# Optimization experiments

Hardware: AMD Instinct MI355X
Metric: run time of the kernel (lower is better)

The kernel has to match this reference:

```python
import jax, jax.numpy as jnp
import numpy as np

DIM = 768
HEADS = 12
HEAD_DIM = DIM // HEADS
B, N = 8, 1024


def setup_inputs() -> dict:
    key = jax.random.key(0)
    ks = jax.random.split(key, 5)
    x = jax.random.normal(ks[0], (B, N, DIM), dtype=jnp.float32)
    shared_rel_pos = jax.random.normal(ks[1], (HEADS, N, N), dtype=jnp.float32)
    qkv_w = jax.random.normal(ks[2], (3 * DIM, DIM), dtype=jnp.float32) * (DIM ** -0.5)
    proj_w = jax.random.normal(ks[3], (DIM, DIM), dtype=jnp.float32) * (DIM ** -0.5)
    proj_b = jnp.zeros((DIM,), dtype=jnp.float32)
    return {"x": x, "shared_rel_pos": shared_rel_pos, "qkv_w": qkv_w,
            "proj_w": proj_w, "proj_b": proj_b}


def reference(x, shared_rel_pos, qkv_w, proj_w, proj_b):
    Bt, Nt, C = x.shape
    scale = HEAD_DIM ** -0.5
    # qkv: Linear(dim, 3*dim, bias=False) -> (B, N, 3, H, hd) -> (3, B, H, N, hd)
    qkv = jnp.einsum('bnc,oc->bno', x, qkv_w)
    qkv = qkv.reshape(Bt, Nt, 3, HEADS, HEAD_DIM).transpose(2, 0, 3, 1, 4)
    q, k, v = qkv[0], qkv[1], qkv[2]
    # scaled dot-product attention with shared relative-position bias
    attn = jnp.einsum('bhqd,bhkd->bhqk', q, k) * scale
    attn = attn + shared_rel_pos[None]  # broadcast over batch
    attn = jax.nn.softmax(attn, axis=-1)
    out = jnp.einsum('bhqk,bhkd->bhqd', attn, v)
    out = out.transpose(0, 2, 1, 3).reshape(Bt, Nt, C)
    return jnp.einsum('bnc,oc->bno', out, proj_w) + proj_b
```

## Files before the change

kernel.cpp:

```cpp
#include <hip/hip_runtime.h>
#include <hip/hip_bf16.h>
#include <stdint.h>

#define HEADS 12
#define HD 64
#define SEQ 1024
#define CDIM 768

typedef __attribute__((ext_vector_type(8))) short bfrag;
typedef __attribute__((ext_vector_type(4))) float facc;
typedef __attribute__((ext_vector_type(4))) _Float16 h4;

__device__ __forceinline__ ushort f2bf(float f) {
    union { float f; uint32_t u; } v; v.f = f;
    uint32_t u = v.u;
    uint32_t r = (u + 0x7FFFu + ((u >> 16) & 1u)) >> 16;
    return (ushort)r;
}
__device__ __forceinline__ ushort f2h(float f) {
    union { _Float16 h; ushort u; } c; c.h = (_Float16)f; return c.u;
}
__device__ __forceinline__ float h2f(uint32_t u16) {
    union { _Float16 h; ushort u; } c; c.u = (ushort)u16; return (float)c.h;
}

__global__ void cvt_all(const float* __restrict__ x, const float* __restrict__ qw,
                        const float* __restrict__ pw, const float* __restrict__ rel,
                        ushort* __restrict__ xd, ushort* __restrict__ qd,
                        ushort* __restrict__ pd, ushort* __restrict__ rd) {
    long i = ((long)blockIdx.x * 256 + threadIdx.x) * 4;
    if (i < 6291456) {
        float4 v = *(const float4*)(x + i);
        ushort4 o = {f2bf(v.x), f2bf(v.y), f2bf(v.z), f2bf(v.w)};
        *(ushort4*)(xd + i) = o;
    } else if (i < 8060928) {
        long j = i - 6291456;
        float4 v = *(const float4*)(qw + j);
        ushort4 o = {f2bf(v.x), f2bf(v.y), f2bf(v.z), f2bf(v.w)};
        *(ushort4*)(qd + j) = o;
    } else if (i < 8650752) {
        long j = i - 8060928;
        float4 v = *(const float4*)(pw + j);
        ushort4 o = {f2bf(v.x), f2bf(v.y), f2bf(v.z), f2bf(v.w)};
        *(ushort4*)(pd + j) = o;
    } else {
        long j = i - 8650752;
        float4 v = *(const float4*)(rel + j);
        ushort4 o = {f2h(v.x * 1.44269504f), f2h(v.y * 1.44269504f),
                     f2h(v.z * 1.44269504f), f2h(v.w * 1.44269504f)};
        *(ushort4*)(rd + j) = o;
    }
}

#define GLOAD16(gsrc, ldst) \
    __builtin_amdgcn_global_load_lds((const __attribute__((address_space(1))) uint32_t*)(gsrc), \
                                     (__attribute__((address_space(3))) uint32_t*)(ldst), 16, 0, 0)

template<int EPI>
__global__ __launch_bounds__(256) void gemm_nt(
    const ushort* __restrict__ A, const ushort* __restrict__ Bm,
    ushort* __restrict__ qb, ushort* __restrict__ kb, ushort* __restrict__ vb,
    const float* __restrict__ projb, float* __restrict__ out)
{
    __shared__ ushort As[128 * 32];
    __shared__ ushort Bs[128 * 32];
    const int t = threadIdx.x;
    const int w = t >> 6, l = t & 63;
    const int wm = w >> 1, wn = w & 1;
    const int lr = l & 15, lg = l >> 4;
    const int m0 = blockIdx.x * 128;
    const int o0 = blockIdx.y * 128;

    facc acc[4][4] = {};

    const int srow = w * 16 + (l >> 2);
    const int scol = (l & 3) * 8;
    const ushort* Ag = A + (size_t)(m0 + srow) * CDIM + scol;
    const ushort* Bg = Bm + (size_t)(o0 + srow) * CDIM + scol;

    for (int k0 = 0; k0 < CDIM; k0 += 32) {
        __syncthreads();
        GLOAD16(Ag + k0,             As + w * 512);
        GLOAD16(Ag + 64 * CDIM + k0, As + 2048 + w * 512);
        GLOAD16(Bg + k0,             Bs + w * 512);
        GLOAD16(Bg + 64 * CDIM + k0, Bs + 2048 + w * 512);
        __syncthreads();
        bfrag af[4], bf[4];
#pragma unroll
        for (int m = 0; m < 4; ++m)
            af[m] = *(const bfrag*)&As[(wm * 64 + m * 16 + lr) * 32 + lg * 8];
#pragma unroll
        for (int n = 0; n < 4; ++n)
            bf[n] = *(const bfrag*)&Bs[(wn * 64 + n * 16 + lr) * 32 + lg * 8];
#pragma unroll
        for (int m = 0; m < 4; ++m)
#pragma unroll
            for (int n = 0; n < 4; ++n)
                acc[m][n] = __builtin_amdgcn_mfma_f32_16x16x32_bf16(af[m], bf[n], acc[m][n], 0, 0, 0);
    }

    if (EPI == 0) {
        const int tsel = o0 / CDIM;
        const int h_base = (o0 % CDIM) / 64;
        ushort* dst = (tsel == 0) ? qb : ((tsel == 1) ? kb : vb);
        const float scl = (tsel == 0) ? 0.18033688f : 1.0f;
#pragma unroll
        for (int m = 0; m < 4; ++m) {
            int grow = m0 + wm * 64 + m * 16 + lg * 4;
#pragma unroll
            for (int n = 0; n < 4; ++n) {
                int h = h_base + wn;
                int d = n * 16 + lr;
#pragma unroll
                for (int r = 0; r < 4; ++r) {
                    int row = grow + r;
                    int b = row >> 10, nn = row & 1023;
                    ushort val = (tsel == 2) ? f2h(acc[m][n][r])
                                             : f2bf(acc[m][n][r] * scl);
                    dst[(((size_t)(b * HEADS + h)) * SEQ + nn) * HD + d] = val;
                }
            }
        }
    } else {
#pragma unroll
        for (int m = 0; m < 4; ++m) {
            int grow = m0 + wm * 64 + m * 16 + lg * 4;
#pragma unroll
            for (int n = 0; n < 4; ++n) {
                int o = o0 + wn * 64 + n * 16 + lr;
                float bias = projb[o];
#pragma unroll
                for (int r = 0; r < 4; ++r)
                    out[(size_t)(grow + r) * CDIM + o] = acc[m][n][r] + bias;
            }
        }
    }
}

__global__ __launch_bounds__(256, 3) void attn_kernel(
    const ushort* __restrict__ qbuf, const ushort* __restrict__ kbuf,
    const ushort* __restrict__ vbuf, const ushort* __restrict__ biash,
    ushort* __restrict__ attn_out)
{
    __shared__ ushort Ks[2][64 * 72];
    __shared__ ushort Vt[2][64 * 72];

    const int t = threadIdx.x;
    const int w = t >> 6, l = t & 63;
    const int lr = l & 15, lg = l >> 4;

    const int bid = blockIdx.x;
    const int lid = (bid & 7) * 96 + (bid >> 3);
    const int h  = lid >> 6;
    const int qt = (lid >> 3) & 7;
    const int b  = lid & 7;

    const int q0 = qt * 128;
    const size_t headoff = (size_t)(b * HEADS + h) * SEQ * HD;
    const int qrb = q0 + w * 32;

    bfrag aQ[2][2];
#pragma unroll
    for (int n = 0; n < 2; ++n) {
        const ushort* Qp = qbuf + headoff + (size_t)(qrb + n * 16 + lr) * HD;
        aQ[n][0] = *(const bfrag*)(Qp + lg * 8);
        aQ[n][1] = *(const bfrag*)(Qp + 32 + lg * 8);
    }

    float mrun[2] = {-1e30f, -1e30f}, lrun[2] = {0.0f, 0.0f};
    facc Ov[2][4] = {};

    const ushort* bprow[2];
#pragma unroll
    for (int n = 0; n < 2; ++n)
        bprow[n] = biash + ((size_t)h * SEQ + qrb + n * 16 + lr) * SEQ;

    const int krow = t >> 3, kc = (t & 7) * 8;
    const int p2 = t & 31, vg_ = t >> 5;
    const ushort* kgb = kbuf + headoff + (size_t)krow * HD + kc;
    const ushort* vgb = vbuf + headoff + (size_t)(2 * p2) * HD + vg_ * 8;

    bfrag krA = *(const bfrag*)(kgb);
    bfrag krB = *(const bfrag*)(kgb + (size_t)32 * HD);
    bfrag vrA = *(const bfrag*)(vgb);
    bfrag vrB = *(const bfrag*)(vgb + HD);
    uint2 bcur[2][4], bnxt[2][4];
#pragma unroll
    for (int n = 0; n < 2; ++n)
#pragma unroll
        for (int c = 0; c < 4; ++c)
            bcur[n][c] = *(const uint2*)(bprow[n] + c * 16 + lg * 4);

    *(bfrag*)&Ks[0][krow * 72 + kc] = krA;
    *(bfrag*)&Ks[0][(krow + 32) * 72 + kc] = krB;
#pragma unroll
    for (int i = 0; i < 8; ++i) {
        uint32_t pk = (uint32_t)(uint16_t)vrA[i] | ((uint32_t)(uint16_t)vrB[i] << 16);
        *(uint32_t*)&Vt[0][(vg_ * 8 + i) * 72 + 2 * p2] = pk;
    }
    krA = *(const bfrag*)(kgb + (size_t)64 * HD);
    krB = *(const bfrag*)(kgb + (size_t)96 * HD);
    vrA = *(const bfrag*)(vgb + (size_t)64 * HD);
    vrB = *(const bfrag*)(vgb + (size_t)65 * HD);
    __syncthreads();

    for (int tt = 0; tt < 16; ++tt) {
        const int cur = tt & 1;
        const ushort* Kc = Ks[cur];
        const ushort* Vc = Vt[cur];

        facc St[2][4];
        __builtin_amdgcn_s_setprio(1);
#pragma unroll
        for (int c = 0; c < 4; ++c) {
            bfrag kf0 = *(const bfrag*)&Kc[(c * 16 + lr) * 72 + lg * 8];
            bfrag kf1 = *(const bfrag*)&Kc[(c * 16 + lr) * 72 + 32 + lg * 8];
#pragma unroll
            for (int n = 0; n < 2; ++n) {
                uint2 bb = bcur[n][c];
                facc s;
                s[0] = h2f(bb.x & 0xffffu);
                s[1] = h2f(bb.x >> 16);
                s[2] = h2f(bb.y & 0xffffu);
                s[3] = h2f(bb.y >> 16);
                s = __builtin_amdgcn_mfma_f32_16x16x32_bf16(kf0, aQ[n][0], s, 0, 0, 0);
                s = __builtin_amdgcn_mfma_f32_16x16x32_bf16(kf1, aQ[n][1], s, 0, 0, 0);
                St[n][c] = s;
            }
        }
        __builtin_amdgcn_s_setprio(0);

        if (tt < 15) {
            const int kvn = (tt + 1) << 6;
#pragma unroll
            for (int n = 0; n < 2; ++n)
#pragma unroll
                for (int c = 0; c < 4; ++c)
                    bnxt[n][c] = *(const uint2*)(bprow[n] + kvn + c * 16 + lg * 4);
        }

        float pmax[2];
#pragma unroll
        for (int n = 0; n < 2; ++n) {
            float m0 = fmaxf(fmaxf(St[n][0][0], St[n][0][1]), fmaxf(St[n][0][2], St[n][0][3]));
            float m1 = fmaxf(fmaxf(St[n][1][0], St[n][1][1]), fmaxf(St[n][1][2], St[n][1][3]));
            float m2 = fmaxf(fmaxf(St[n][2][0], St[n][2][1]), fmaxf(St[n][2][2], St[n][2][3]));
            float m3 = fmaxf(fmaxf(St[n][3][0], St[n][3][1]), fmaxf(St[n][3][2], St[n][3][3]));
            float mx = fmaxf(fmaxf(m0, m1), fmaxf(m2, m3));
            mx = fmaxf(mx, __shfl_xor(mx, 16));
            mx = fmaxf(mx, __shfl_xor(mx, 32));
            pmax[n] = mx;
        }

        int ok = (pmax[0] <= mrun[0] + 11.541560f) && (pmax[1] <= mrun[1] + 11.541560f);
        if (!__all(ok)) {
            float al[2];
#pragma unroll
            for (int n = 0; n < 2; ++n) {
                float mnew = fmaxf(mrun[n], pmax[n]);
                al[n] = exp2f(mrun[n] - mnew);
                mrun[n] = mnew;
                lrun[n] *= al[n];
            }
#pragma unroll
            for (int n = 0; n < 2; ++n)
#pragma unroll
                for (int r = 0; r < 4; ++r) {
                    float a = __shfl(al[n], lg * 4 + r);
#pragma unroll
                    for (int d = 0; d < 4; ++d) Ov[n][d][r] *= a;
                }
        }

        h4 pf[2][4];
#pragma unroll
        for (int n = 0; n < 2; ++n) {
            float sum = 0.0f;
#pragma unroll
            for (int c = 0; c < 4; ++c) {
#pragma unroll
                for (int r = 0; r < 4; ++r) {
                    float p = exp2f(St[n][c][r] - mrun[n]);
                    sum += p;
                    pf[n][c][r] = (_Float16)p;
                }
            }
            sum += __shfl_xor(sum, 16);
            sum += __shfl_xor(sum, 32);
            lrun[n] += sum;
        }

        if (tt < 15) {
            *(bfrag*)&Ks[cur ^ 1][krow * 72 + kc] = krA;
            *(bfrag*)&Ks[cur ^ 1][(krow + 32) * 72 + kc] = krB;
#pragma unroll
            for (int i = 0; i < 8; ++i) {
                uint32_t pk = (uint32_t)(uint16_t)vrA[i] | ((uint32_t)(uint16_t)vrB[i] << 16);
                *(uint32_t*)&Vt[cur ^ 1][(vg_ * 8 + i) * 72 + 2 * p2] = pk;
            }
        }
        if (tt < 14) {
            const int kvn = (tt + 2) << 6;
            krA = *(const bfrag*)(kgb + (size_t)kvn * HD);
            krB = *(const bfrag*)(kgb + (size_t)(kvn + 32) * HD);
            vrA = *(const bfrag*)(vgb + (size_t)kvn * HD);
            vrB = *(const bfrag*)(vgb + (size_t)(kvn + 1) * HD);
        }

        __builtin_amdgcn_s_setprio(1);
#pragma unroll
        for (int d0 = 0; d0 < 4; ++d0) {
#pragma unroll
            for (int c = 0; c < 4; ++c) {
                h4 bv = *(const h4*)&Vc[(d0 * 16 + lr) * 72 + c * 16 + lg * 4];
#pragma unroll
                for (int n = 0; n < 2; ++n)
                    Ov[n][d0] = __builtin_amdgcn_mfma_f32_16x16x16f16(pf[n][c], bv, Ov[n][d0], 0, 0, 0);
            }
        }
        __builtin_amdgcn_s_setprio(0);

        if (tt < 15) {
            __syncthreads();
#pragma unroll
            for (int n = 0; n < 2; ++n)
#pragma unroll
                for (int c = 0; c < 4; ++c)
                    bcur[n][c] = bnxt[n][c];
        }
    }

#pragma unroll
    for (int n = 0; n < 2; ++n) {
        ushort* op = attn_out + ((size_t)b * SEQ + qrb + n * 16) * CDIM + h * HD;
#pragma unroll
        for (int r = 0; r < 4; ++r) {
            float ll = __shfl(lrun[n], lg * 4 + r);
            float rl = 1.0f / ll;
#pragma unroll
            for (int d = 0; d < 4; ++d)
                op[(size_t)(lg * 4 + r) * CDIM + d * 16 + lr] = f2bf(Ov[n][d][r] * rl);
        }
    }
}

extern "C" void kernel_launch(void* const* d_in, const int* in_sizes, int n_in,
                              void* d_out, int out_size, void* d_ws, size_t ws_size,
                              hipStream_t stream) {
    const float* x     = (const float*)d_in[0];
    const float* rel   = (const float*)d_in[1];
    const float* qkvw  = (const float*)d_in[2];
    const float* projw = (const float*)d_in[3];
    const float* projb = (const float*)d_in[4];
    float* out = (float*)d_out;

    char* ws = (char*)d_ws;
    ushort* biash = (ushort*)(ws);
    ushort* qb    = (ushort*)(ws + 25165824);
    ushort* kb    = (ushort*)(ws + 37748736);
    ushort* vb    = (ushort*)(ws + 50331648);
    ushort* attnb = (ushort*)(ws + 62914560);
    ushort* xbf   = attnb;
    ushort* wbf   = (ushort*)(ws + 75497472);
    ushort* pwbf  = (ushort*)(ws + 79036416);

    cvt_all<<<20736, 256, 0, stream>>>(x, qkvw, projw, rel, xbf, wbf, pwbf, biash);

    gemm_nt<0><<<dim3(64, 18), 256, 0, stream>>>(xbf, wbf, qb, kb, vb, nullptr, nullptr);
    attn_kernel<<<768, 256, 0, stream>>>(qb, kb, vb, biash, attnb);
    gemm_nt<1><<<dim3(64, 6), 256, 0, stream>>>(attnb, pwbf, nullptr, nullptr, nullptr, projb, out);
}
```

Baseline: 155.2 us.

## Halve attention query tile per block and compute softmax speculatively inline

The attention kernel drops from 128 to 64 query rows per block, with each wave handling 16 rows instead of 32. The grid doubles to 1536 blocks and the launch bound allows 4 blocks per CU. Exponentials are now computed right after each score MFMA using the old running max, and are recomputed only when the max grows past the threshold. This aims to cut register pressure, raise occupancy and overlap exp work with MFMA. In exchange, each K/V tile loaded into LDS is reused by half as many query rows, so K/V traffic doubles.

```diff
diff --git a/kernel.cpp b/kernel.cpp
--- a/kernel.cpp
+++ b/kernel.cpp
@@ -137,7 +137,7 @@
     }
 }
 
-__global__ __launch_bounds__(256, 3) void attn_kernel(
+__global__ __launch_bounds__(256, 4) void attn_kernel(
     const ushort* __restrict__ qbuf, const ushort* __restrict__ kbuf,
     const ushort* __restrict__ vbuf, const ushort* __restrict__ biash,
     ushort* __restrict__ attn_out)
@@ -150,30 +150,26 @@
     const int lr = l & 15, lg = l >> 4;
 
     const int bid = blockIdx.x;
-    const int lid = (bid & 7) * 96 + (bid >> 3);
-    const int h  = lid >> 6;
-    const int qt = (lid >> 3) & 7;
+    const int lid = (bid & 7) * 192 + (bid >> 3);
+    const int h  = lid >> 7;
+    const int qt = (lid >> 3) & 15;
     const int b  = lid & 7;
 
-    const int q0 = qt * 128;
+    const int q0 = qt * 64;
     const size_t headoff = (size_t)(b * HEADS + h) * SEQ * HD;
-    const int qrb = q0 + w * 32;
-
-    bfrag aQ[2][2];
-#pragma unroll
-    for (int n = 0; n < 2; ++n) {
-        const ushort* Qp = qbuf + headoff + (size_t)(qrb + n * 16 + lr) * HD;
-        aQ[n][0] = *(const bfrag*)(Qp + lg * 8);
-        aQ[n][1] = *(const bfrag*)(Qp + 32 + lg * 8);
-    }
-
-    float mrun[2] = {-1e30f, -1e30f}, lrun[2] = {0.0f, 0.0f};
-    facc Ov[2][4] = {};
-
-    const ushort* bprow[2];
-#pragma unroll
-    for (int n = 0; n < 2; ++n)
-        bprow[n] = biash + ((size_t)h * SEQ + qrb + n * 16 + lr) * SEQ;
+    const int qrb = q0 + w * 16;
+
+    bfrag aQ0, aQ1;
+    {
+        const ushort* Qp = qbuf + headoff + (size_t)(qrb + lr) * HD;
+        aQ0 = *(const bfrag*)(Qp + lg * 8);
+        aQ1 = *(const bfrag*)(Qp + 32 + lg * 8);
+    }
+
+    float mrun = -1e30f, lrun = 0.0f;
+    facc Ov[4] = {};
+
+    const ushort* bprow = biash + ((size_t)h * SEQ + qrb + lr) * SEQ;
 
     const int krow = t >> 3, kc = (t & 7) * 8;
     const int p2 = t & 31, vg_ = t >> 5;
@@ -184,12 +180,10 @@
     bfrag krB = *(const bfrag*)(kgb + (size_t)32 * HD);
     bfrag vrA = *(const bfrag*)(vgb);
     bfrag vrB = *(const bfrag*)(vgb + HD);
-    uint2 bcur[2][4], bnxt[2][4];
-#pragma unroll
-    for (int n = 0; n < 2; ++n)
-#pragma unroll
-        for (int c = 0; c < 4; ++c)
-            bcur[n][c] = *(const uint2*)(bprow[n] + c * 16 + lg * 4);
+    uint2 bcur[4], bnxt[4];
+#pragma unroll
+    for (int c = 0; c < 4; ++c)
+        bcur[c] = *(const uint2*)(bprow + c * 16 + lg * 4);
 
     *(bfrag*)&Ks[0][krow * 72 + kc] = krA;
     *(bfrag*)&Ks[0][(krow + 32) * 72 + kc] = krB;
@@ -209,86 +203,66 @@
         const ushort* Kc = Ks[cur];
         const ushort* Vc = Vt[cur];
 
-        facc St[2][4];
-        __builtin_amdgcn_s_setprio(1);
+        facc St[4];
+        h4 pf[4];
+        float psum = 0.0f, pmax = -3.0e38f;
 #pragma unroll
         for (int c = 0; c < 4; ++c) {
             bfrag kf0 = *(const bfrag*)&Kc[(c * 16 + lr) * 72 + lg * 8];
             bfrag kf1 = *(const bfrag*)&Kc[(c * 16 + lr) * 72 + 32 + lg * 8];
-#pragma unroll
-            for (int n = 0; n < 2; ++n) {
-                uint2 bb = bcur[n][c];
-                facc s;
-                s[0] = h2f(bb.x & 0xffffu);
-                s[1] = h2f(bb.x >> 16);
-                s[2] = h2f(bb.y & 0xffffu);
-                s[3] = h2f(bb.y >> 16);
-                s = __builtin_amdgcn_mfma_f32_16x16x32_bf16(kf0, aQ[n][0], s, 0, 0, 0);
-                s = __builtin_amdgcn_mfma_f32_16x16x32_bf16(kf1, aQ[n][1], s, 0, 0, 0);
-                St[n][c] = s;
-            }
-        }
-        __builtin_amdgcn_s_setprio(0);
+            uint2 bb = bcur[c];
+            facc s;
+            s[0] = h2f(bb.x & 0xffffu);
+            s[1] = h2f(bb.x >> 16);
+            s[2] = h2f(bb.y & 0xffffu);
+            s[3] = h2f(bb.y >> 16);
+            __builtin_amdgcn_s_setprio(1);
+            s = __builtin_amdgcn_mfma_f32_16x16x32_bf16(kf0, aQ0, s, 0, 0, 0);
+            s = __builtin_amdgcn_mfma_f32_16x16x32_bf16(kf1, aQ1, s, 0, 0, 0);
+            __builtin_amdgcn_s_setprio(0);
+            St[c] = s;
+#pragma unroll
+            for (int r = 0; r < 4; ++r) {
+                float p = exp2f(s[r] - mrun);
+                psum += p;
+                pf[c][r] = (_Float16)p;
+                pmax = fmaxf(pmax, s[r]);
+            }
+        }
 
         if (tt < 15) {
             const int kvn = (tt + 1) << 6;
 #pragma unroll
-            for (int n = 0; n < 2; ++n)
-#pragma unroll
-                for (int c = 0; c < 4; ++c)
-                    bnxt[n][c] = *(const uint2*)(bprow[n] + kvn + c * 16 + lg * 4);
-        }
-
-        float pmax[2];
-#pragma unroll
-        for (int n = 0; n < 2; ++n) {
-            float m0 = fmaxf(fmaxf(St[n][0][0], St[n][0][1]), fmaxf(St[n][0][2], St[n][0][3]));
-            float m1 = fmaxf(fmaxf(St[n][1][0], St[n][1][1]), fmaxf(St[n][1][2], St[n][1][3]));
-            float m2 = fmaxf(fmaxf(St[n][2][0], St[n][2][1]), fmaxf(St[n][2][2], St[n][2][3]));
-            float m3 = fmaxf(fmaxf(St[n][3][0], St[n][3][1]), fmaxf(St[n][3][2], St[n][3][3]));
-            float mx = fmaxf(fmaxf(m0, m1), fmaxf(m2, m3));
-            mx = fmaxf(mx, __shfl_xor(mx, 16));
-            mx = fmaxf(mx, __shfl_xor(mx, 32));
-            pmax[n] = mx;
-        }
-
-        int ok = (pmax[0] <= mrun[0] + 11.541560f) && (pmax[1] <= mrun[1] + 11.541560f);
-        if (!__all(ok)) {
-            float al[2];
-#pragma unroll
-            for (int n = 0; n < 2; ++n) {
-                float mnew = fmaxf(mrun[n], pmax[n]);
-                al[n] = exp2f(mrun[n] - mnew);
-                mrun[n] = mnew;
-                lrun[n] *= al[n];
-            }
-#pragma unroll
-            for (int n = 0; n < 2; ++n)
+            for (int c = 0; c < 4; ++c)
+                bnxt[c] = *(const uint2*)(bprow + kvn + c * 16 + lg * 4);
+        }
+
+        pmax = fmaxf(pmax, __shfl_xor(pmax, 16));
+        pmax = fmaxf(pmax, __shfl_xor(pmax, 32));
+        if (!__all(pmax <= mrun + 11.541560f)) {
+            float mnew = fmaxf(mrun, pmax);
+            float al = exp2f(mrun - mnew);
+            psum = 0.0f;
+#pragma unroll
+            for (int c = 0; c < 4; ++c)
 #pragma unroll
                 for (int r = 0; r < 4; ++r) {
-                    float a = __shfl(al[n], lg * 4 + r);
-#pragma unroll
-                    for (int d = 0; d < 4; ++d) Ov[n][d][r] *= a;
+                    float p = exp2f(St[c][r] - mnew);
+                    psum += p;
+                    pf[c][r] = (_Float16)p;
                 }
-        }
-
-        h4 pf[2][4];
-#pragma unroll
-        for (int n = 0; n < 2; ++n) {
-            float sum = 0.0f;
-#pragma unroll
-            for (int c = 0; c < 4; ++c) {
-#pragma unroll
-                for (int r = 0; r < 4; ++r) {
-                    float p = exp2f(St[n][c][r] - mrun[n]);
-                    sum += p;
-                    pf[n][c][r] = (_Float16)p;
-                }
-            }
-            sum += __shfl_xor(sum, 16);
-            sum += __shfl_xor(sum, 32);
-            lrun[n] += sum;
-        }
+#pragma unroll
+            for (int r = 0; r < 4; ++r) {
+                float a = __shfl(al, lg * 4 + r);
+#pragma unroll
+                for (int d = 0; d < 4; ++d) Ov[d][r] *= a;
+            }
+            lrun *= al;
+            mrun = mnew;
+        }
+        psum += __shfl_xor(psum, 16);
+        psum += __shfl_xor(psum, 32);
+        lrun += psum;
 
         if (tt < 15) {
             *(bfrag*)&Ks[cur ^ 1][krow * 72 + kc] = krA;
@@ -313,9 +287,7 @@
 #pragma unroll
             for (int c = 0; c < 4; ++c) {
                 h4 bv = *(const h4*)&Vc[(d0 * 16 + lr) * 72 + c * 16 + lg * 4];
-#pragma unroll
-                for (int n = 0; n < 2; ++n)
-                    Ov[n][d0] = __builtin_amdgcn_mfma_f32_16x16x16f16(pf[n][c], bv, Ov[n][d0], 0, 0, 0);
+                Ov[d0] = __builtin_amdgcn_mfma_f32_16x16x16f16(pf[c], bv, Ov[d0], 0, 0, 0);
             }
         }
         __builtin_amdgcn_s_setprio(0);
@@ -323,24 +295,19 @@
         if (tt < 15) {
             __syncthreads();
 #pragma unroll
-            for (int n = 0; n < 2; ++n)
-#pragma unroll
-                for (int c = 0; c < 4; ++c)
-                    bcur[n][c] = bnxt[n][c];
-        }
-    }
-
-#pragma unroll
-    for (int n = 0; n < 2; ++n) {
-        ushort* op = attn_out + ((size_t)b * SEQ + qrb + n * 16) * CDIM + h * HD;
-#pragma unroll
-        for (int r = 0; r < 4; ++r) {
-            float ll = __shfl(lrun[n], lg * 4 + r);
-            float rl = 1.0f / ll;
-#pragma unroll
-            for (int d = 0; d < 4; ++d)
-                op[(size_t)(lg * 4 + r) * CDIM + d * 16 + lr] = f2bf(Ov[n][d][r] * rl);
-        }
+            for (int c = 0; c < 4; ++c)
+                bcur[c] = bnxt[c];
+        }
+    }
+
+    ushort* op = attn_out + ((size_t)b * SEQ + qrb) * CDIM + h * HD;
+#pragma unroll
+    for (int r = 0; r < 4; ++r) {
+        float ll = __shfl(lrun, lg * 4 + r);
+        float rl = 1.0f / ll;
+#pragma unroll
+        for (int d = 0; d < 4; ++d)
+            op[(size_t)(lg * 4 + r) * CDIM + d * 16 + lr] = f2bf(Ov[d][r] * rl);
     }
 }
 
@@ -367,6 +334,6 @@
     cvt_all<<<20736, 256, 0, stream>>>(x, qkvw, projw, rel, xbf, wbf, pwbf, biash);
 
     gemm_nt<0><<<dim3(64, 18), 256, 0, stream>>>(xbf, wbf, qb, kb, vb, nullptr, nullptr);
-    attn_kernel<<<768, 256, 0, stream>>>(qb, kb, vb, biash, attnb);
+    attn_kernel<<<1536, 256, 0, stream>>>(qb, kb, vb, biash, attnb);
     gemm_nt<1><<<dim3(64, 6), 256, 0, stream>>>(attnb, pwbf, nullptr, nullptr, nullptr, projb, out);
 }
```

Result: slower. 164.0 us (+5.7%).

## Read fp32 bias directly in attention and fuse exp into score loop

Applied to the files above, without the earlier changes.

Drops the separate fp32-to-fp16 conversion pass over the relative-position bias, so the attention kernel reads fp32 bias directly and scales by log2e inline. This removes one write and one re-read of the bias tensor, but the attention kernel now reads twice as many bias bytes and holds more bias registers. The exponentials and row sums are computed speculatively inside the QK loop using the old running max, and recomputed only when the max grows past a threshold. Probabilities are packed to fp16 with the pkrtz conversion, and the prefetch double-buffer for bias is collapsed to a single buffer.

```diff
diff --git a/kernel.cpp b/kernel.cpp
--- a/kernel.cpp
+++ b/kernel.cpp
@@ -6,10 +6,12 @@
 #define HD 64
 #define SEQ 1024
 #define CDIM 768
+#define LOG2E 1.44269504f
 
 typedef __attribute__((ext_vector_type(8))) short bfrag;
 typedef __attribute__((ext_vector_type(4))) float facc;
 typedef __attribute__((ext_vector_type(4))) _Float16 h4;
+typedef __attribute__((ext_vector_type(2))) __fp16 pk2;
 
 __device__ __forceinline__ ushort f2bf(float f) {
     union { float f; uint32_t u; } v; v.f = f;
@@ -20,14 +22,17 @@
 __device__ __forceinline__ ushort f2h(float f) {
     union { _Float16 h; ushort u; } c; c.h = (_Float16)f; return c.u;
 }
-__device__ __forceinline__ float h2f(uint32_t u16) {
-    union { _Float16 h; ushort u; } c; c.u = (ushort)u16; return (float)c.h;
+__device__ __forceinline__ h4 pack4h(float p0, float p1, float p2, float p3) {
+    union { h4 v4; pk2 v2[2]; } u;
+    u.v2[0] = __builtin_amdgcn_cvt_pkrtz(p0, p1);
+    u.v2[1] = __builtin_amdgcn_cvt_pkrtz(p2, p3);
+    return u.v4;
 }
 
 __global__ void cvt_all(const float* __restrict__ x, const float* __restrict__ qw,
-                        const float* __restrict__ pw, const float* __restrict__ rel,
+                        const float* __restrict__ pw,
                         ushort* __restrict__ xd, ushort* __restrict__ qd,
-                        ushort* __restrict__ pd, ushort* __restrict__ rd) {
+                        ushort* __restrict__ pd) {
     long i = ((long)blockIdx.x * 256 + threadIdx.x) * 4;
     if (i < 6291456) {
         float4 v = *(const float4*)(x + i);
@@ -43,12 +48,6 @@
         float4 v = *(const float4*)(pw + j);
         ushort4 o = {f2bf(v.x), f2bf(v.y), f2bf(v.z), f2bf(v.w)};
         *(ushort4*)(pd + j) = o;
-    } else {
-        long j = i - 8650752;
-        float4 v = *(const float4*)(rel + j);
-        ushort4 o = {f2h(v.x * 1.44269504f), f2h(v.y * 1.44269504f),
-                     f2h(v.z * 1.44269504f), f2h(v.w * 1.44269504f)};
-        *(ushort4*)(rd + j) = o;
     }
 }
 
@@ -139,7 +138,7 @@
 
 __global__ __launch_bounds__(256, 3) void attn_kernel(
     const ushort* __restrict__ qbuf, const ushort* __restrict__ kbuf,
-    const ushort* __restrict__ vbuf, const ushort* __restrict__ biash,
+    const ushort* __restrict__ vbuf, const float* __restrict__ biasf,
     ushort* __restrict__ attn_out)
 {
     __shared__ ushort Ks[2][64 * 72];
@@ -170,10 +169,10 @@
     float mrun[2] = {-1e30f, -1e30f}, lrun[2] = {0.0f, 0.0f};
     facc Ov[2][4] = {};
 
-    const ushort* bprow[2];
+    const float* bprow[2];
 #pragma unroll
     for (int n = 0; n < 2; ++n)
-        bprow[n] = biash + ((size_t)h * SEQ + qrb + n * 16 + lr) * SEQ;
+        bprow[n] = biasf + ((size_t)h * SEQ + qrb + n * 16 + lr) * SEQ;
 
     const int krow = t >> 3, kc = (t & 7) * 8;
     const int p2 = t & 31, vg_ = t >> 5;
@@ -184,12 +183,12 @@
     bfrag krB = *(const bfrag*)(kgb + (size_t)32 * HD);
     bfrag vrA = *(const bfrag*)(vgb);
     bfrag vrB = *(const bfrag*)(vgb + HD);
-    uint2 bcur[2][4], bnxt[2][4];
+    float4 bcur[2][4];
 #pragma unroll
     for (int n = 0; n < 2; ++n)
 #pragma unroll
         for (int c = 0; c < 4; ++c)
-            bcur[n][c] = *(const uint2*)(bprow[n] + c * 16 + lg * 4);
+            bcur[n][c] = *(const float4*)(bprow[n] + c * 16 + lg * 4);
 
     *(bfrag*)&Ks[0][krow * 72 + kc] = krA;
     *(bfrag*)&Ks[0][(krow + 32) * 72 + kc] = krB;
@@ -210,25 +209,33 @@
         const ushort* Vc = Vt[cur];
 
         facc St[2][4];
-        __builtin_amdgcn_s_setprio(1);
+        h4 pf[2][4];
+        float psum[2] = {0.0f, 0.0f};
+        float pmax[2] = {-3.0e38f, -3.0e38f};
 #pragma unroll
         for (int c = 0; c < 4; ++c) {
             bfrag kf0 = *(const bfrag*)&Kc[(c * 16 + lr) * 72 + lg * 8];
             bfrag kf1 = *(const bfrag*)&Kc[(c * 16 + lr) * 72 + 32 + lg * 8];
 #pragma unroll
             for (int n = 0; n < 2; ++n) {
-                uint2 bb = bcur[n][c];
+                float4 bb = bcur[n][c];
                 facc s;
-                s[0] = h2f(bb.x & 0xffffu);
-                s[1] = h2f(bb.x >> 16);
-                s[2] = h2f(bb.y & 0xffffu);
-                s[3] = h2f(bb.y >> 16);
+                s[0] = bb.x * LOG2E; s[1] = bb.y * LOG2E;
+                s[2] = bb.z * LOG2E; s[3] = bb.w * LOG2E;
+                __builtin_amdgcn_s_setprio(1);
                 s = __builtin_amdgcn_mfma_f32_16x16x32_bf16(kf0, aQ[n][0], s, 0, 0, 0);
                 s = __builtin_amdgcn_mfma_f32_16x16x32_bf16(kf1, aQ[n][1], s, 0, 0, 0);
+                __builtin_amdgcn_s_setprio(0);
                 St[n][c] = s;
-            }
-        }
-        __builtin_amdgcn_s_setprio(0);
+                float p0 = exp2f(s[0] - mrun[n]);
+                float p1 = exp2f(s[1] - mrun[n]);
+                float p2f = exp2f(s[2] - mrun[n]);
+                float p3 = exp2f(s[3] - mrun[n]);
+                psum[n] += (p0 + p1) + (p2f + p3);
+                pmax[n] = fmaxf(pmax[n], fmaxf(fmaxf(s[0], s[1]), fmaxf(s[2], s[3])));
+                pf[n][c] = pack4h(p0, p1, p2f, p3);
+            }
+        }
 
         if (tt < 15) {
             const int kvn = (tt + 1) << 6;
@@ -236,58 +243,45 @@
             for (int n = 0; n < 2; ++n)
 #pragma unroll
                 for (int c = 0; c < 4; ++c)
-                    bnxt[n][c] = *(const uint2*)(bprow[n] + kvn + c * 16 + lg * 4);
-        }
-
-        float pmax[2];
+                    bcur[n][c] = *(const float4*)(bprow[n] + kvn + c * 16 + lg * 4);
+        }
+
 #pragma unroll
         for (int n = 0; n < 2; ++n) {
-            float m0 = fmaxf(fmaxf(St[n][0][0], St[n][0][1]), fmaxf(St[n][0][2], St[n][0][3]));
-            float m1 = fmaxf(fmaxf(St[n][1][0], St[n][1][1]), fmaxf(St[n][1][2], St[n][1][3]));
-            float m2 = fmaxf(fmaxf(St[n][2][0], St[n][2][1]), fmaxf(St[n][2][2], St[n][2][3]));
-            float m3 = fmaxf(fmaxf(St[n][3][0], St[n][3][1]), fmaxf(St[n][3][2], St[n][3][3]));
-            float mx = fmaxf(fmaxf(m0, m1), fmaxf(m2, m3));
-            mx = fmaxf(mx, __shfl_xor(mx, 16));
-            mx = fmaxf(mx, __shfl_xor(mx, 32));
-            pmax[n] = mx;
-        }
-
+            pmax[n] = fmaxf(pmax[n], __shfl_xor(pmax[n], 16));
+            pmax[n] = fmaxf(pmax[n], __shfl_xor(pmax[n], 32));
+        }
         int ok = (pmax[0] <= mrun[0] + 11.541560f) && (pmax[1] <= mrun[1] + 11.541560f);
         if (!__all(ok)) {
-            float al[2];
 #pragma unroll
             for (int n = 0; n < 2; ++n) {
                 float mnew = fmaxf(mrun[n], pmax[n]);
-                al[n] = exp2f(mrun[n] - mnew);
-                mrun[n] = mnew;
-                lrun[n] *= al[n];
-            }
-#pragma unroll
-            for (int n = 0; n < 2; ++n)
+                float al = exp2f(mrun[n] - mnew);
+                psum[n] = 0.0f;
+#pragma unroll
+                for (int c = 0; c < 4; ++c) {
+                    float p0 = exp2f(St[n][c][0] - mnew);
+                    float p1 = exp2f(St[n][c][1] - mnew);
+                    float p2f = exp2f(St[n][c][2] - mnew);
+                    float p3 = exp2f(St[n][c][3] - mnew);
+                    psum[n] += (p0 + p1) + (p2f + p3);
+                    pf[n][c] = pack4h(p0, p1, p2f, p3);
+                }
 #pragma unroll
                 for (int r = 0; r < 4; ++r) {
-                    float a = __shfl(al[n], lg * 4 + r);
+                    float a = __shfl(al, lg * 4 + r);
 #pragma unroll
                     for (int d = 0; d < 4; ++d) Ov[n][d][r] *= a;
                 }
-        }
-
-        h4 pf[2][4];
+                lrun[n] *= al;
+                mrun[n] = mnew;
+            }
+        }
 #pragma unroll
         for (int n = 0; n < 2; ++n) {
-            float sum = 0.0f;
-#pragma unroll
-            for (int c = 0; c < 4; ++c) {
-#pragma unroll
-                for (int r = 0; r < 4; ++r) {
-                    float p = exp2f(St[n][c][r] - mrun[n]);
-                    sum += p;
-                    pf[n][c][r] = (_Float16)p;
-                }
-            }
-            sum += __shfl_xor(sum, 16);
-            sum += __shfl_xor(sum, 32);
-            lrun[n] += sum;
+            psum[n] += __shfl_xor(psum[n], 16);
+            psum[n] += __shfl_xor(psum[n], 32);
+            lrun[n] += psum[n];
         }
 
         if (tt < 15) {
@@ -320,14 +314,7 @@
         }
         __builtin_amdgcn_s_setprio(0);
 
-        if (tt < 15) {
-            __syncthreads();
-#pragma unroll
-            for (int n = 0; n < 2; ++n)
-#pragma unroll
-                for (int c = 0; c < 4; ++c)
-                    bcur[n][c] = bnxt[n][c];
-        }
+        if (tt < 15) __syncthreads();
     }
 
 #pragma unroll
@@ -355,18 +342,17 @@
     float* out = (float*)d_out;
 
     char* ws = (char*)d_ws;
-    ushort* biash = (ushort*)(ws);
-    ushort* qb    = (ushort*)(ws + 25165824);
-    ushort* kb    = (ushort*)(ws + 37748736);
-    ushort* vb    = (ushort*)(ws + 50331648);
-    ushort* attnb = (ushort*)(ws + 62914560);
+    ushort* qb    = (ushort*)(ws);
+    ushort* kb    = (ushort*)(ws + 12582912);
+    ushort* vb    = (ushort*)(ws + 25165824);
+    ushort* attnb = (ushort*)(ws + 37748736);
     ushort* xbf   = attnb;
-    ushort* wbf   = (ushort*)(ws + 75497472);
-    ushort* pwbf  = (ushort*)(ws + 79036416);
-
-    cvt_all<<<20736, 256, 0, stream>>>(x, qkvw, projw, rel, xbf, wbf, pwbf, biash);
+    ushort* wbf   = (ushort*)(ws + 50331648);
+    ushort* pwbf  = (ushort*)(ws + 53870592);
+
+    cvt_all<<<8448, 256, 0, stream>>>(x, qkvw, projw, xbf, wbf, pwbf);
 
     gemm_nt<0><<<dim3(64, 18), 256, 0, stream>>>(xbf, wbf, qb, kb, vb, nullptr, nullptr);
-    attn_kernel<<<768, 256, 0, stream>>>(qb, kb, vb, biash, attnb);
+    attn_kernel<<<768, 256, 0, stream>>>(qb, kb, vb, rel, attnb);
     gemm_nt<1><<<dim3(64, 6), 256, 0, stream>>>(attnb, pwbf, nullptr, nullptr, nullptr, projb, out);
 }
```

Measured after the change: 148.8 us. 1.04x faster.
